# Kernel optimization log

Measured on AMD Instinct MI355X. Metric: run time of the kernel, lower is better.

The kernel has to match this reference:

```python
import jax, jax.numpy as jnp
import numpy as np

DIM = 1024
HEADS = 16
DIM_HEAD = 64


def setup_inputs() -> dict:
    key = jax.random.key(0)
    k1, k2 = jax.random.split(key)
    x = jax.random.normal(k1, (2, 2048, DIM), dtype=jnp.float32)
    # to_qkv: Linear(dim, 3*heads*dim_head, bias=False); torch weight is [out,in],
    # we store the transposed [in,out] form for x @ W.
    W_qkv = jax.random.normal(k2, (DIM, 3 * HEADS * DIM_HEAD), dtype=jnp.float32) * (DIM ** -0.5)
    return {"x": x, "W_qkv": W_qkv}


def reference(x, W_qkv):
    b, n, _ = x.shape
    h, d = HEADS, DIM_HEAD
    scale = d ** -0.5
    qkv = x @ W_qkv                              # [b, n, 3*h*d]
    q, k, v = jnp.split(qkv, 3, axis=-1)
    # 'b n (h d) -> b h n d'
    q = q.reshape(b, n, h, d).transpose(0, 2, 1, 3)
    k = k.reshape(b, n, h, d).transpose(0, 2, 1, 3)
    v = v.reshape(b, n, h, d).transpose(0, 2, 1, 3)
    dots = jnp.einsum('bhnd,bhmd->bhnm', q, k) * scale
    attn = jax.nn.softmax(dots, axis=-1)
    out = jnp.einsum('bhnm,bhmd->bhnd', attn, v)
    out = out.transpose(0, 2, 1, 3).reshape(b, n, h * d)  # 'b h n d -> b n (h d)'
    return out + x  # residual (to_out is never applied in the source forward)
```

## Files before the change

### kernel.cpp

```cpp
#include <hip/hip_runtime.h>

#define DIM   1024
#define NQKV  3072
#define SEQ   2048
#define HEADS 16
#define DHEAD 64
#define M_TOT 4096

typedef __bf16 bf16;
typedef __bf16 bf16x8 __attribute__((ext_vector_type(8)));
typedef float  f32x4  __attribute__((ext_vector_type(4)));

typedef const __attribute__((address_space(1))) unsigned int gu32;
typedef __attribute__((address_space(3))) unsigned int su32;

static __device__ __forceinline__ unsigned short f2b(float f) {
    bf16 h = (bf16)f;
    return __builtin_bit_cast(unsigned short, h);
}

#define CAST_BLOCKS (M_TOT * DIM / (256 * 4))
#define TR_NB (NQKV / 64)
__global__ void prep_kernel(const float* __restrict__ x,
                            unsigned short* __restrict__ xb,
                            const float* __restrict__ W,
                            unsigned short* __restrict__ Wt) {
    __shared__ float tile[64][65];
    const int id  = blockIdx.x;
    const int tid = threadIdx.x;
    if (id < CAST_BLOCKS) {
        int i = (id * 256 + tid) * 4;
        float4 v = *(const float4*)(x + i);
        ushort4 o;
        o.x = f2b(v.x); o.y = f2b(v.y); o.z = f2b(v.z); o.w = f2b(v.w);
        *(ushort4*)(xb + i) = o;
    } else {
        int t  = id - CAST_BLOCKS;
        int nb = t % TR_NB;
        int kb = t / TR_NB;
        #pragma unroll
        for (int p = 0; p < 4; p++) {
            int kl = p * 16 + (tid >> 4);
            int nl = (tid & 15) * 4;
            float4 v = *(const float4*)&W[(size_t)(kb * 64 + kl) * NQKV + nb * 64 + nl];
            tile[nl + 0][kl] = v.x;
            tile[nl + 1][kl] = v.y;
            tile[nl + 2][kl] = v.z;
            tile[nl + 3][kl] = v.w;
        }
        __syncthreads();
        #pragma unroll
        for (int p = 0; p < 2; p++) {
            int nl = p * 32 + (tid >> 3);
            int k8 = (tid & 7) * 8;
            int n  = nb * 64 + nl;
            float s = (n < 1024) ? 0.18033688f : 1.0f;
            float4 a = *(const float4*)&tile[nl][k8];
            float4 b = *(const float4*)&tile[nl][k8 + 4];
            ushort4 o0, o1;
            o0.x = f2b(a.x * s); o0.y = f2b(a.y * s); o0.z = f2b(a.z * s); o0.w = f2b(a.w * s);
            o1.x = f2b(b.x * s); o1.y = f2b(b.y * s); o1.z = f2b(b.z * s); o1.w = f2b(b.w * s);
            uint4 pk;
            pk.x = ((unsigned)o0.y << 16) | o0.x;
            pk.y = ((unsigned)o0.w << 16) | o0.z;
            pk.z = ((unsigned)o1.y << 16) | o1.x;
            pk.w = ((unsigned)o1.w << 16) | o1.z;
            *(uint4*)&Wt[(size_t)n * DIM + kb * 64 + k8] = pk;
        }
    }
}

#define LDC 136
__global__ __launch_bounds__(256, 2) void qkv_gemm_kernel(
    const unsigned short* __restrict__ A,
    const unsigned short* __restrict__ Bt,
    unsigned short* __restrict__ Qw,
    unsigned short* __restrict__ Kw,
    unsigned short* __restrict__ Vtw)
{
    __shared__ __align__(16) unsigned char smem[49152];
    unsigned short* As = (unsigned short*)smem;
    unsigned short* Bs = (unsigned short*)(smem + 32768);
    unsigned short* Cs = (unsigned short*)smem;

    const int tid  = threadIdx.x;
    const int m0   = blockIdx.y * 256;
    const int n0   = blockIdx.x * 128;
    const int w    = tid >> 6;
    const int lane = tid & 63;
    const int l16  = lane & 15;
    const int quad = lane >> 4;
    const int wm   = (w >> 1) * 128;
    const int wn   = (w & 1) * 64;
    const int srow = lane >> 3;
    const int scol = ((lane & 7) ^ srow) * 8;
    const int xa   = l16 & 7;

    f32x4 acc[8][4];
    const f32x4 fzero = {0.f, 0.f, 0.f, 0.f};
    #pragma unroll
    for (int i = 0; i < 8; i++)
        #pragma unroll
        for (int j = 0; j < 4; j++) acc[i][j] = fzero;

    const unsigned short* Ag = A  + (size_t)(m0 + w * 64 + srow) * DIM + scol;
    const unsigned short* Bg = Bt + (size_t)(n0 + w * 32 + srow) * DIM + scol;

    for (int ki = 0; ki < 16; ki++) {
        const int kt = ki * 64;
        if (ki > 0) __syncthreads();
        #pragma unroll
        for (int j = 0; j < 8; j++)
            __builtin_amdgcn_global_load_lds((gu32*)(Ag + kt + (size_t)j * 8 * DIM),
                                             (su32*)&As[(w * 64 + j * 8) * 64], 16, 0, 0);
        #pragma unroll
        for (int j = 0; j < 4; j++)
            __builtin_amdgcn_global_load_lds((gu32*)(Bg + kt + (size_t)j * 8 * DIM),
                                             (su32*)&Bs[(w * 32 + j * 8) * 64], 16, 0, 0);
        __syncthreads();

        #pragma unroll
        for (int s = 0; s < 2; s++) {
            const int col = ((s * 4 + quad) ^ xa) * 8;
            bf16x8 af[8], bfr[4];
            #pragma unroll
            for (int i = 0; i < 8; i++)
                af[i]  = *(const bf16x8*)(&As[(wm + i * 16 + l16) * 64 + col]);
            #pragma unroll
            for (int j = 0; j < 4; j++)
                bfr[j] = *(const bf16x8*)(&Bs[(wn + j * 16 + l16) * 64 + col]);
            #pragma unroll
            for (int i = 0; i < 8; i++)
                #pragma unroll
                for (int j = 0; j < 4; j++)
                    acc[i][j] = __builtin_amdgcn_mfma_f32_16x16x32_bf16(af[i], bfr[j], acc[i][j], 0, 0, 0);
        }
    }
    __syncthreads();

    const int part = n0 >> 10;
    const int h0   = (n0 & 1023) >> 6;

    if (part < 2) {
        unsigned short* dst = (part == 0) ? Qw : Kw;
        #pragma unroll
        for (int half = 0; half < 2; half++) {
            if (half) __syncthreads();
            if ((w >> 1) == half) {
                #pragma unroll
                for (int i = 0; i < 8; i++)
                    #pragma unroll
                    for (int j = 0; j < 4; j++)
                        #pragma unroll
                        for (int r = 0; r < 4; r++)
                            Cs[(i * 16 + quad * 4 + r) * LDC + wn + j * 16 + l16] = f2b(acc[i][j][r]);
            }
            __syncthreads();
            const int mg  = m0 + half * 128;
            const int b   = mg >> 11;
            const int npb = mg & 2047;
            #pragma unroll
            for (int pass = 0; pass < 8; pass++) {
                int mi = pass * 16 + (tid >> 4);
                int ci = (tid & 15) * 8;
                uint4 v = *(const uint4*)&Cs[mi * LDC + ci];
                int bh = b * HEADS + h0 + (ci >> 6);
                *(uint4*)&dst[((size_t)bh * SEQ + npb + mi) * DHEAD + (ci & 63)] = v;
            }
        }
    } else {
        #pragma unroll
        for (int half = 0; half < 2; half++) {
            if (half) __syncthreads();
            if ((w >> 1) == half) {
                #pragma unroll
                for (int i = 0; i < 8; i++)
                    #pragma unroll
                    for (int j = 0; j < 4; j++) {
                        ushort4 pk;
                        pk.x = f2b(acc[i][j][0]); pk.y = f2b(acc[i][j][1]);
                        pk.z = f2b(acc[i][j][2]); pk.w = f2b(acc[i][j][3]);
                        *(ushort4*)&Cs[(wn + j * 16 + l16) * LDC + i * 16 + quad * 4] = pk;
                    }
            }
            __syncthreads();
            const int mg  = m0 + half * 128;
            const int b   = mg >> 11;
            const int npb = mg & 2047;
            #pragma unroll
            for (int pass = 0; pass < 8; pass++) {
                int ci = pass * 16 + (tid >> 4);
                int mi = (tid & 15) * 8;
                uint4 v = *(const uint4*)&Cs[ci * LDC + mi];
                int bh = b * HEADS + h0 + (ci >> 6);
                *(uint4*)&Vtw[((size_t)bh * DHEAD + (ci & 63)) * SEQ + npb + mi] = v;
            }
        }
    }
}

__global__ __launch_bounds__(512, 2) void attn_kernel(
    const unsigned short* __restrict__ Qw,
    const unsigned short* __restrict__ Kw,
    const unsigned short* __restrict__ Vtw,
    const float* __restrict__ x,
    float* __restrict__ out)
{
    __shared__ __align__(16) unsigned char smem[65536];
    unsigned short* base = (unsigned short*)smem;
    float* scratch = (float*)smem;

    const int id  = blockIdx.x;
    const int qt  = id >> 5;
    const int bh  = ((id & 7) << 2) | ((id >> 3) & 3);
    const int tid = threadIdx.x;
    const int w   = tid >> 6, lane = tid & 63;
    const int l16 = lane & 15, quad = lane >> 4;
    const int g   = w & 3;
    const int p   = w >> 2;
    const int xq  = l16 & 7;

    const unsigned short* Qb = Qw + ((size_t)bh * SEQ + qt * 256 + g * 64 + l16) * DHEAD;
    bf16x8 qf[4][2];
    #pragma unroll
    for (int qh = 0; qh < 4; qh++) {
        qf[qh][0] = *(const bf16x8*)(Qb + qh * 16 * DHEAD + quad * 8);
        qf[qh][1] = *(const bf16x8*)(Qb + qh * 16 * DHEAD + 32 + quad * 8);
    }

    bf16x8 ones;
    #pragma unroll
    for (int j = 0; j < 8; j++) ones[j] = (bf16)1.0f;

    f32x4 o[4][4], dsum[4];
    const f32x4 fzero = {0.f, 0.f, 0.f, 0.f};
    #pragma unroll
    for (int qh = 0; qh < 4; qh++) {
        #pragma unroll
        for (int d = 0; d < 4; d++) o[qh][d] = fzero;
        dsum[qh] = fzero;
    }

    const unsigned short* Kg = Kw  + (size_t)bh * SEQ * DHEAD;
    const unsigned short* Vg = Vtw + (size_t)bh * DHEAD * SEQ;

    const int sl   = lane >> 3;
    const int c16s = (lane & 7) ^ sl;
    const int pr   = 8 * w + sl;
    const int rlog = ((pr >> 2) & 3) * 8 + ((pr >> 4) & 1) * 4 + (pr & 3) + (pr & 32);
    const size_t koff = (size_t)rlog * DHEAD + c16s * 8;
    const size_t voff = (size_t)pr * SEQ + c16s * 8;

    __builtin_amdgcn_global_load_lds((gu32*)(Kg + koff), (su32*)(base + w * 512), 16, 0, 0);
    __builtin_amdgcn_global_load_lds((gu32*)(Vg + voff), (su32*)(base + 4096 + w * 512), 16, 0, 0);
    __syncthreads();

    for (int t = 0; t < 32; t++) {
        const int cur = t & 1, nxt = cur ^ 1;
        if (t + 1 < 32) {
            const size_t kb = (size_t)((t + 1) * 64) * DHEAD;
            const int kv = (t + 1) * 64;
            __builtin_amdgcn_global_load_lds((gu32*)(Kg + kb + koff),
                                             (su32*)(base + nxt * 8192 + w * 512), 16, 0, 0);
            __builtin_amdgcn_global_load_lds((gu32*)(Vg + voff + kv),
                                             (su32*)(base + nxt * 8192 + 4096 + w * 512), 16, 0, 0);
        }

        const unsigned short* Kb = base + cur * 8192;
        const unsigned short* Vb = base + cur * 8192 + 4096;

        f32x4 sacc[4][2];
        #pragma unroll
        for (int qh = 0; qh < 4; qh++)
            #pragma unroll
            for (int ki = 0; ki < 2; ki++) sacc[qh][ki] = fzero;
        #pragma unroll
        for (int s = 0; s < 2; s++) {
            const int col = ((s * 4 + quad) ^ xq) * 8;
            #pragma unroll
            for (int ki = 0; ki < 2; ki++) {
                bf16x8 kf = *(const bf16x8*)(&Kb[(p * 32 + ki * 16 + l16) * 64 + col]);
                #pragma unroll
                for (int qh = 0; qh < 4; qh++)
                    sacc[qh][ki] = __builtin_amdgcn_mfma_f32_16x16x32_bf16(kf, qf[qh][s], sacc[qh][ki], 0, 0, 0);
            }
        }

        bf16x8 pf[4];
        #pragma unroll
        for (int qh = 0; qh < 4; qh++)
            #pragma unroll
            for (int ki = 0; ki < 2; ki++)
                #pragma unroll
                for (int r = 0; r < 4; r++)
                    pf[qh][ki * 4 + r] = (bf16)__builtin_amdgcn_exp2f(sacc[qh][ki][r]);

        const int colv = ((p * 4 + quad) ^ xq) * 8;
        #pragma unroll
        for (int qh = 0; qh < 4; qh++)
            dsum[qh] = __builtin_amdgcn_mfma_f32_16x16x32_bf16(pf[qh], ones, dsum[qh], 0, 0, 0);
        #pragma unroll
        for (int d = 0; d < 4; d++) {
            bf16x8 vf = *(const bf16x8*)(&Vb[(d * 16 + l16) * 64 + colv]);
            #pragma unroll
            for (int qh = 0; qh < 4; qh++)
                o[qh][d] = __builtin_amdgcn_mfma_f32_16x16x32_bf16(pf[qh], vf, o[qh][d], 0, 0, 0);
        }
        __syncthreads();
    }

    #pragma unroll
    for (int ch = 0; ch < 2; ch++) {
        if (ch) __syncthreads();
        if (p == 1) {
            float* sc = scratch + ((size_t)(g * 64 + lane)) * 40;
            #pragma unroll
            for (int q2 = 0; q2 < 2; q2++) {
                int qh = ch * 2 + q2;
                #pragma unroll
                for (int di = 0; di < 4; di++)
                    *(f32x4*)(sc + q2 * 20 + di * 4) = o[qh][di];
                *(f32x4*)(sc + q2 * 20 + 16) = dsum[qh];
            }
        }
        __syncthreads();
        if (p == 0) {
            float* sc = scratch + ((size_t)(g * 64 + lane)) * 40;
            #pragma unroll
            for (int q2 = 0; q2 < 2; q2++) {
                int qh = ch * 2 + q2;
                #pragma unroll
                for (int di = 0; di < 4; di++)
                    o[qh][di] += *(const f32x4*)(sc + q2 * 20 + di * 4);
                dsum[qh] += *(const f32x4*)(sc + q2 * 20 + 16);
            }
        }
    }

    if (p == 0) {
        const int b = bh >> 4, h = bh & 15;
        #pragma unroll
        for (int qh = 0; qh < 4; qh++) {
            float lr[4];
            #pragma unroll
            for (int r = 0; r < 4; r++) lr[r] = __builtin_amdgcn_rcpf(dsum[qh][r]);
            #pragma unroll
            for (int di = 0; di < 4; di++)
                #pragma unroll
                for (int r = 0; r < 4; r++) {
                    int np  = qt * 256 + g * 64 + qh * 16 + quad * 4 + r;
                    int col = h * 64 + di * 16 + l16;
                    size_t gidx = ((size_t)(b * SEQ + np)) * DIM + col;
                    out[gidx] = o[qh][di][r] * lr[r] + x[gidx];
                }
        }
    }
}

extern "C" void kernel_launch(void* const* d_in, const int* in_sizes, int n_in,
                              void* d_out, int out_size, void* d_ws, size_t ws_size,
                              hipStream_t stream) {
    const float* x  = (const float*)d_in[0];
    const float* Wq = (const float*)d_in[1];
    float* out = (float*)d_out;

    unsigned short* xb = (unsigned short*)d_ws;
    unsigned short* Wt = xb + (size_t)M_TOT * DIM;
    unsigned short* Qw = Wt + (size_t)NQKV * DIM;
    unsigned short* Kw = Qw + (size_t)32 * SEQ * DHEAD;
    unsigned short* Vt = Kw + (size_t)32 * SEQ * DHEAD;

    prep_kernel<<<CAST_BLOCKS + TR_NB * (DIM / 64), 256, 0, stream>>>(x, xb, Wq, Wt);
    qkv_gemm_kernel<<<dim3(NQKV / 128, M_TOT / 256), 256, 0, stream>>>(xb, Wt, Qw, Kw, Vt);
    attn_kernel<<<(SEQ / 256) * 32, 512, 0, stream>>>(Qw, Kw, Vt, x, out);
}
```

Before: 145.8 us.

## Halve attention block to 4 waves with 128-query tiles and MFMA priority hints

The attention kernel now uses 256-thread blocks over 128-query tiles instead of 512 threads over 256 queries, so the grid doubles and the LDS footprint is halved. Each wave issues two K/V async LDS loads per tile instead of one, so the 64-key double buffer is still filled. s_setprio is raised around the QK and PV MFMA sections so the wave doing matrix math gets issue priority over waves doing exp and loads. The cost is that each K/V tile is now fetched by twice as many blocks, which adds L2 traffic.

Result: slower. 261.0 us (+79.0%).

```diff
diff --git a/kernel.cpp b/kernel.cpp
--- a/kernel.cpp
+++ b/kernel.cpp
@@ -199,14 +199,14 @@
     }
 }
 
-__global__ __launch_bounds__(512, 2) void attn_kernel(
+__global__ __launch_bounds__(256, 4) void attn_kernel(
     const unsigned short* __restrict__ Qw,
     const unsigned short* __restrict__ Kw,
     const unsigned short* __restrict__ Vtw,
     const float* __restrict__ x,
     float* __restrict__ out)
 {
-    __shared__ __align__(16) unsigned char smem[65536];
+    __shared__ __align__(16) unsigned char smem[32768];
     unsigned short* base = (unsigned short*)smem;
     float* scratch = (float*)smem;
 
@@ -216,11 +216,11 @@
     const int tid = threadIdx.x;
     const int w   = tid >> 6, lane = tid & 63;
     const int l16 = lane & 15, quad = lane >> 4;
-    const int g   = w & 3;
-    const int p   = w >> 2;
+    const int g   = w & 1;
+    const int p   = w >> 1;
     const int xq  = l16 & 7;
 
-    const unsigned short* Qb = Qw + ((size_t)bh * SEQ + qt * 256 + g * 64 + l16) * DHEAD;
+    const unsigned short* Qb = Qw + ((size_t)bh * SEQ + qt * 128 + g * 64 + l16) * DHEAD;
     bf16x8 qf[4][2];
     #pragma unroll
     for (int qh = 0; qh < 4; qh++) {
@@ -246,13 +246,20 @@
 
     const int sl   = lane >> 3;
     const int c16s = (lane & 7) ^ sl;
-    const int pr   = 8 * w + sl;
-    const int rlog = ((pr >> 2) & 3) * 8 + ((pr >> 4) & 1) * 4 + (pr & 3) + (pr & 32);
-    const size_t koff = (size_t)rlog * DHEAD + c16s * 8;
-    const size_t voff = (size_t)pr * SEQ + c16s * 8;
-
-    __builtin_amdgcn_global_load_lds((gu32*)(Kg + koff), (su32*)(base + w * 512), 16, 0, 0);
-    __builtin_amdgcn_global_load_lds((gu32*)(Vg + voff), (su32*)(base + 4096 + w * 512), 16, 0, 0);
+    int pr[2], rlog[2];
+    #pragma unroll
+    for (int c = 0; c < 2; c++) {
+        pr[c]   = w * 16 + c * 8 + sl;
+        rlog[c] = ((pr[c] >> 2) & 3) * 8 + ((pr[c] >> 4) & 1) * 4 + (pr[c] & 3) + (pr[c] & 32);
+    }
+
+    #pragma unroll
+    for (int c = 0; c < 2; c++) {
+        __builtin_amdgcn_global_load_lds((gu32*)(Kg + (size_t)rlog[c] * DHEAD + c16s * 8),
+                                         (su32*)(base + w * 1024 + c * 512), 16, 0, 0);
+        __builtin_amdgcn_global_load_lds((gu32*)(Vg + (size_t)pr[c] * SEQ + c16s * 8),
+                                         (su32*)(base + 4096 + w * 1024 + c * 512), 16, 0, 0);
+    }
     __syncthreads();
 
     for (int t = 0; t < 32; t++) {
@@ -260,10 +267,13 @@
         if (t + 1 < 32) {
             const size_t kb = (size_t)((t + 1) * 64) * DHEAD;
             const int kv = (t + 1) * 64;
-            __builtin_amdgcn_global_load_lds((gu32*)(Kg + kb + koff),
-                                             (su32*)(base + nxt * 8192 + w * 512), 16, 0, 0);
-            __builtin_amdgcn_global_load_lds((gu32*)(Vg + voff + kv),
-                                             (su32*)(base + nxt * 8192 + 4096 + w * 512), 16, 0, 0);
+            #pragma unroll
+            for (int c = 0; c < 2; c++) {
+                __builtin_amdgcn_global_load_lds((gu32*)(Kg + kb + (size_t)rlog[c] * DHEAD + c16s * 8),
+                                                 (su32*)(base + nxt * 8192 + w * 1024 + c * 512), 16, 0, 0);
+                __builtin_amdgcn_global_load_lds((gu32*)(Vg + (size_t)pr[c] * SEQ + kv + c16s * 8),
+                                                 (su32*)(base + nxt * 8192 + 4096 + w * 1024 + c * 512), 16, 0, 0);
+            }
         }
 
         const unsigned short* Kb = base + cur * 8192;
@@ -274,6 +284,7 @@
         for (int qh = 0; qh < 4; qh++)
             #pragma unroll
             for (int ki = 0; ki < 2; ki++) sacc[qh][ki] = fzero;
+        __builtin_amdgcn_s_setprio(1);
         #pragma unroll
         for (int s = 0; s < 2; s++) {
             const int col = ((s * 4 + quad) ^ xq) * 8;
@@ -285,6 +296,7 @@
                     sacc[qh][ki] = __builtin_amdgcn_mfma_f32_16x16x32_bf16(kf, qf[qh][s], sacc[qh][ki], 0, 0, 0);
             }
         }
+        __builtin_amdgcn_s_setprio(0);
 
         bf16x8 pf[4];
         #pragma unroll
@@ -296,6 +308,7 @@
                     pf[qh][ki * 4 + r] = (bf16)__builtin_amdgcn_exp2f(sacc[qh][ki][r]);
 
         const int colv = ((p * 4 + quad) ^ xq) * 8;
+        __builtin_amdgcn_s_setprio(1);
         #pragma unroll
         for (int qh = 0; qh < 4; qh++)
             dsum[qh] = __builtin_amdgcn_mfma_f32_16x16x32_bf16(pf[qh], ones, dsum[qh], 0, 0, 0);
@@ -306,6 +319,7 @@
             for (int qh = 0; qh < 4; qh++)
                 o[qh][d] = __builtin_amdgcn_mfma_f32_16x16x32_bf16(pf[qh], vf, o[qh][d], 0, 0, 0);
         }
+        __builtin_amdgcn_s_setprio(0);
         __syncthreads();
     }
 
@@ -348,7 +362,7 @@
             for (int di = 0; di < 4; di++)
                 #pragma unroll
                 for (int r = 0; r < 4; r++) {
-                    int np  = qt * 256 + g * 64 + qh * 16 + quad * 4 + r;
+                    int np  = qt * 128 + g * 64 + qh * 16 + quad * 4 + r;
                     int col = h * 64 + di * 16 + l16;
                     size_t gidx = ((size_t)(b * SEQ + np)) * DIM + col;
                     out[gidx] = o[qh][di][r] * lr[r] + x[gidx];
@@ -372,5 +386,5 @@
 
     prep_kernel<<<CAST_BLOCKS + TR_NB * (DIM / 64), 256, 0, stream>>>(x, xb, Wq, Wt);
     qkv_gemm_kernel<<<dim3(NQKV / 128, M_TOT / 256), 256, 0, stream>>>(xb, Wt, Qw, Kw, Vt);
-    attn_kernel<<<(SEQ / 256) * 32, 512, 0, stream>>>(Qw, Kw, Vt, x, out);
-}
+    attn_kernel<<<(SEQ / 128) * 32, 256, 0, stream>>>(Qw, Kw, Vt, x, out);
+}
```
